# Kernel optimization log

Measured on AMD Instinct MI355X. Metric: run time of the kernel, lower is better.

The kernel has to match this reference:

```python
import jax, jax.numpy as jnp
import numpy as np

N = 100000   # nodes
E = 600000   # edges
F = 128      # input features
H = 128      # hidden size
A = 64       # n_actions
G = 64       # number of graphs in batch
L = 3        # GAT layers
EPS = 1e-5   # GraphNorm eps


def setup_inputs() -> dict:
    key = jax.random.key(0)
    ks = jax.random.split(key, 8)
    x = jax.random.normal(ks[0], (N, F), dtype=jnp.float32)
    edge_index = jax.random.randint(ks[1], (2, E), 0, N, dtype=jnp.int64)
    batch = jnp.sort(jax.random.randint(ks[2], (N,), 0, G, dtype=jnp.int64))
    Ws = jax.random.normal(ks[3], (L, H, H), dtype=jnp.float32) * (1.0 / np.sqrt(H))
    att_src = jax.random.normal(ks[4], (L, H), dtype=jnp.float32) * 0.1
    att_dst = jax.random.normal(ks[5], (L, H), dtype=jnp.float32) * 0.1
    conv_bias = jnp.zeros((L, H), dtype=jnp.float32)
    gn_weight = jnp.ones((L - 1, H), dtype=jnp.float32)
    gn_bias = jnp.zeros((L - 1, H), dtype=jnp.float32)
    gn_mean_scale = jnp.ones((L - 1, H), dtype=jnp.float32)
    W1 = jax.random.normal(ks[6], (H, H), dtype=jnp.float32) * (1.0 / np.sqrt(H))
    b1 = jnp.zeros((H,), dtype=jnp.float32)
    W2 = jax.random.normal(ks[7], (H, A), dtype=jnp.float32) * (1.0 / np.sqrt(H))
    b2 = jnp.zeros((A,), dtype=jnp.float32)
    return dict(x=x, edge_index=edge_index, batch=batch, Ws=Ws, att_src=att_src,
                att_dst=att_dst, conv_bias=conv_bias, gn_weight=gn_weight,
                gn_bias=gn_bias, gn_mean_scale=gn_mean_scale,
                W1=W1, b1=b1, W2=W2, b2=b2)


def reference(x, edge_index, batch, Ws, att_src, att_dst, conv_bias,
              gn_weight, gn_bias, gn_mean_scale, W1, b1, W2, b2):
    src, dst = edge_index[0], edge_index[1]
    n = x.shape[0]
    h = x
    for l in range(L):
        # GATConv (heads=1, add_self_loops=False): h' = W h, edge attention
        hW = h @ Ws[l]                              # [N,H]
        a_s = hW @ att_src[l]                       # [N]
        a_d = hW @ att_dst[l]                       # [N]
        e = jax.nn.leaky_relu(a_s[src] + a_d[dst], 0.2)      # [E]
        m = jax.ops.segment_max(e, dst, num_segments=n)      # stable softmax per dst
        ex = jnp.exp(e - m[dst])
        s = jax.ops.segment_sum(ex, dst, num_segments=n)
        alpha = ex / (s[dst] + 1e-16)               # PyG softmax eps
        h = jax.ops.segment_sum(hW[src] * alpha[:, None], dst, num_segments=n) + conv_bias[l]
        if l < L - 1:
            # GraphNorm with batch=None (source passes no batch to gnn): one graph
            mean = h.mean(axis=0, keepdims=True)
            out = h - mean * gn_mean_scale[l]
            var = (out * out).mean(axis=0, keepdims=True)
            h = gn_weight[l] * out / jnp.sqrt(var + EPS) + gn_bias[l]
            h = jax.nn.leaky_relu(h, 0.01)          # act between layers (not after last)
    pooled = jax.ops.segment_sum(h, batch, num_segments=G)   # global_add_pool [G,H]
    z = jax.nn.leaky_relu(pooled @ W1 + b1, 0.01)
    return z @ W2 + b2                               # [G,A]
```

## Files before the change

kernel.cpp:

```cpp
#include <hip/hip_runtime.h>
#include <math.h>

#define HD 128
#define GG 64
#define CSB 256

typedef __attribute__((ext_vector_type(8))) short short8;
typedef __attribute__((ext_vector_type(4))) float f32x4;

__device__ __forceinline__ float leaky(float x, float s) { return x > 0.f ? x : s * x; }

__device__ __forceinline__ unsigned short bf16_of(float f) {
    union { float f; unsigned u; } v; v.f = f;
    unsigned r = v.u + 0x7fffu + ((v.u >> 16) & 1u);
    return (unsigned short)(r >> 16);
}
__device__ __forceinline__ float f_of_bf16(unsigned short u) {
    union { unsigned u; float f; } v; v.u = ((unsigned)u) << 16;
    return v.f;
}

__device__ __forceinline__ int sw(int row, int chunk) {
    return row * 128 + ((chunk ^ (row & 15)) << 3);
}

__global__ void k_init(const float* __restrict__ Ws, unsigned short* __restrict__ Wt,
                       int* __restrict__ bcnt) {
    int i = blockIdx.x * 256 + threadIdx.x;
    if (i < 3 * 16384) {
        int l = i >> 14, rem = i & 16383;
        int nn = rem >> 7, k = rem & 127;
        Wt[i] = bf16_of(Ws[l * 16384 + k * 128 + nn]);
    }
    if (i < 513) bcnt[i] = 0;
}


__global__ __launch_bounds__(256) void k_gemm_a32(
    const float* __restrict__ A, const unsigned short* __restrict__ Wt,
    const float* __restrict__ att_s, const float* __restrict__ att_d,
    unsigned short* __restrict__ hWb, float* __restrict__ a_s, float* __restrict__ a_d,
    int n) {
    __shared__ unsigned short Bs[128 * 128];
    const int tid = threadIdx.x;
    const int base = blockIdx.x * 64;

    const uint4* Wt4 = (const uint4*)Wt;
    uint4* Bs4 = (uint4*)Bs;
#pragma unroll
    for (int j = 0; j < 8; ++j) {
        int flat = tid + j * 256;
        int col = flat >> 4, c8 = flat & 15;
        Bs4[(col << 4) + (c8 ^ (col & 15))] = Wt4[flat];
    }

    const int wave = tid >> 6, lane = tid & 63;
    const int m16 = lane & 15, quad = lane >> 4;

    short8 af[4];
    {
        int row = base + wave * 16 + m16;
        row = (row < n) ? row : (n - 1);
        const float4* ap = (const float4*)(A + (size_t)row * 128);
#pragma unroll
        for (int kk = 0; kk < 4; ++kk) {
            float4 v0 = ap[kk * 8 + quad * 2];
            float4 v1 = ap[kk * 8 + quad * 2 + 1];
            union { short8 s; unsigned u[4]; } P;
            P.u[0] = (unsigned)bf16_of(v0.x) | ((unsigned)bf16_of(v0.y) << 16);
            P.u[1] = (unsigned)bf16_of(v0.z) | ((unsigned)bf16_of(v0.w) << 16);
            P.u[2] = (unsigned)bf16_of(v1.x) | ((unsigned)bf16_of(v1.y) << 16);
            P.u[3] = (unsigned)bf16_of(v1.z) | ((unsigned)bf16_of(v1.w) << 16);
            af[kk] = P.s;
        }
    }
    __syncthreads();

    f32x4 acc[8];
#pragma unroll
    for (int ct = 0; ct < 8; ++ct) acc[ct] = (f32x4){0.f, 0.f, 0.f, 0.f};
#pragma unroll
    for (int kk = 0; kk < 4; ++kk) {
#pragma unroll
        for (int ct = 0; ct < 8; ++ct) {
            short8 bfr = *(const short8*)&Bs[sw(ct * 16 + m16, kk * 4 + quad)];
            acc[ct] = __builtin_amdgcn_mfma_f32_16x16x32_bf16(af[kk], bfr, acc[ct], 0, 0, 0);
        }
    }

#pragma unroll
    for (int reg = 0; reg < 4; ++reg) {
        int gr = base + wave * 16 + quad * 4 + reg;
        bool ok = gr < n;
        unsigned short* rowp = hWb + (size_t)gr * 128 + m16;
        float s = 0.f, dd = 0.f;
#pragma unroll
        for (int ct = 0; ct < 8; ++ct) {
            float v = acc[ct][reg];
            int col = ct * 16 + m16;
            if (ok) rowp[ct * 16] = bf16_of(v);
            s = fmaf(v, att_s[col], s);
            dd = fmaf(v, att_d[col], dd);
        }
#pragma unroll
        for (int off = 1; off < 16; off <<= 1) {
            s += __shfl_xor(s, off, 64);
            dd += __shfl_xor(dd, off, 64);
        }
        if (m16 == 0 && ok) { a_s[gr] = s; a_d[gr] = dd; }
    }
}

__global__ __launch_bounds__(256) void k_gemm_a16(
    const unsigned short* __restrict__ Ab, const unsigned short* __restrict__ Wt,
    const float* __restrict__ att_s, const float* __restrict__ att_d,
    const float* __restrict__ alpha, const float* __restrict__ beta,
    unsigned short* __restrict__ hWb, float* __restrict__ a_s, float* __restrict__ a_d,
    int n) {
    __shared__ unsigned short Bs[128 * 128];
    const int tid = threadIdx.x;
    const int base = blockIdx.x * 64;

    const uint4* Wt4 = (const uint4*)Wt;
    uint4* Bs4 = (uint4*)Bs;
#pragma unroll
    for (int j = 0; j < 8; ++j) {
        int flat = tid + j * 256;
        int col = flat >> 4, c8 = flat & 15;
        Bs4[(col << 4) + (c8 ^ (col & 15))] = Wt4[flat];
    }

    const int wave = tid >> 6, lane = tid & 63;
    const int m16 = lane & 15, quad = lane >> 4;
    const float4* al4 = (const float4*)alpha;
    const float4* be4 = (const float4*)beta;

    short8 af[4];
    {
        int row = base + wave * 16 + m16;
        row = (row < n) ? row : (n - 1);
        const uint4* ap = (const uint4*)(Ab + (size_t)row * 128);
#pragma unroll
        for (int kk = 0; kk < 4; ++kk) {
            uint4 raw = ap[kk * 4 + quad];
            int c4 = kk * 8 + quad * 2;
            float4 a0 = al4[c4], a1 = al4[c4 + 1];
            float4 b0 = be4[c4], b1 = be4[c4 + 1];
            float f0 = leaky(fmaf(f_of_bf16(raw.x & 0xffff), a0.x, b0.x), 0.01f);
            float f1 = leaky(fmaf(f_of_bf16(raw.x >> 16),    a0.y, b0.y), 0.01f);
            float f2 = leaky(fmaf(f_of_bf16(raw.y & 0xffff), a0.z, b0.z), 0.01f);
            float f3 = leaky(fmaf(f_of_bf16(raw.y >> 16),    a0.w, b0.w), 0.01f);
            float f4 = leaky(fmaf(f_of_bf16(raw.z & 0xffff), a1.x, b1.x), 0.01f);
            float f5 = leaky(fmaf(f_of_bf16(raw.z >> 16),    a1.y, b1.y), 0.01f);
            float f6 = leaky(fmaf(f_of_bf16(raw.w & 0xffff), a1.z, b1.z), 0.01f);
            float f7 = leaky(fmaf(f_of_bf16(raw.w >> 16),    a1.w, b1.w), 0.01f);
            union { short8 s; unsigned u[4]; } P;
            P.u[0] = (unsigned)bf16_of(f0) | ((unsigned)bf16_of(f1) << 16);
            P.u[1] = (unsigned)bf16_of(f2) | ((unsigned)bf16_of(f3) << 16);
            P.u[2] = (unsigned)bf16_of(f4) | ((unsigned)bf16_of(f5) << 16);
            P.u[3] = (unsigned)bf16_of(f6) | ((unsigned)bf16_of(f7) << 16);
            af[kk] = P.s;
        }
    }
    __syncthreads();

    f32x4 acc[8];
#pragma unroll
    for (int ct = 0; ct < 8; ++ct) acc[ct] = (f32x4){0.f, 0.f, 0.f, 0.f};
#pragma unroll
    for (int kk = 0; kk < 4; ++kk) {
#pragma unroll
        for (int ct = 0; ct < 8; ++ct) {
            short8 bfr = *(const short8*)&Bs[sw(ct * 16 + m16, kk * 4 + quad)];
            acc[ct] = __builtin_amdgcn_mfma_f32_16x16x32_bf16(af[kk], bfr, acc[ct], 0, 0, 0);
        }
    }

#pragma unroll
    for (int reg = 0; reg < 4; ++reg) {
        int gr = base + wave * 16 + quad * 4 + reg;
        bool ok = gr < n;
        unsigned short* rowp = hWb + (size_t)gr * 128 + m16;
        float s = 0.f, dd = 0.f;
#pragma unroll
        for (int ct = 0; ct < 8; ++ct) {
            float v = acc[ct][reg];
            int col = ct * 16 + m16;
            if (ok) rowp[ct * 16] = bf16_of(v);
            s = fmaf(v, att_s[col], s);
            dd = fmaf(v, att_d[col], dd);
        }
#pragma unroll
        for (int off = 1; off < 16; off <<= 1) {
            s += __shfl_xor(s, off, 64);
            dd += __shfl_xor(dd, off, 64);
        }
        if (m16 == 0 && ok) { a_s[gr] = s; a_d[gr] = dd; }
    }
}


__global__ __launch_bounds__(256) void k_bcount(const int* __restrict__ dst,
                                                int* __restrict__ bcnt, int e) {
    __shared__ int lh[512];
    const int tid = threadIdx.x;
    for (int t = tid; t < 512; t += 256) lh[t] = 0;
    __syncthreads();
    for (int i = blockIdx.x * 256 + tid; i < e; i += gridDim.x * 256)
        atomicAdd(&lh[dst[i] >> 9], 1);
    __syncthreads();
    for (int t = tid; t < 512; t += 256)
        if (lh[t]) atomicAdd(&bcnt[t], lh[t]);
}

__global__ void k_bscan(const int* __restrict__ bcnt, int* __restrict__ bbase,
                        int* __restrict__ bcur, int* __restrict__ offs,
                        int nbk, int n, int e) {
    __shared__ int s[512];
    int t = threadIdx.x;
    int v = (t < nbk) ? bcnt[t] : 0;
    s[t] = v;
    __syncthreads();
    for (int off = 1; off < 512; off <<= 1) {
        int u = (t >= off) ? s[t - off] : 0;
        __syncthreads();
        s[t] += u;
        __syncthreads();
    }
    if (t < nbk) { bbase[t] = s[t] - v; bcur[t] = s[t] - v; }
    if (t == 0) { bbase[nbk] = e; offs[n] = e; }
}

__global__ __launch_bounds__(256) void k_part(const int* __restrict__ src,
                                              const int* __restrict__ dst,
                                              int* __restrict__ bcur,
                                              int* __restrict__ ebuf, int e) {
    __shared__ int lh[512];
    __shared__ int lbase[512];
    const int tid = threadIdx.x;
    const int chunk = (e + gridDim.x - 1) / gridDim.x;
    const int i0 = blockIdx.x * chunk;
    const int i1 = min(e, i0 + chunk);
    for (int t = tid; t < 512; t += 256) lh[t] = 0;
    __syncthreads();
    for (int i = i0 + tid; i < i1; i += 256) atomicAdd(&lh[dst[i] >> 9], 1);
    __syncthreads();
    for (int t = tid; t < 512; t += 256) {
        int c = lh[t];
        lbase[t] = c ? atomicAdd(&bcur[t], c) : 0;
    }
    __syncthreads();
    for (int t = tid; t < 512; t += 256) lh[t] = 0;
    __syncthreads();
    for (int i = i0 + tid; i < i1; i += 256) {
        int d = dst[i];
        int b = d >> 9;
        int p = lbase[b] + atomicAdd(&lh[b], 1);
        ebuf[p] = ((d & 511) << 18) | src[i];
    }
}

__global__ __launch_bounds__(256) void k_bscatter(const int* __restrict__ ebuf,
                                                  const int* __restrict__ bbase,
                                                  int* __restrict__ offs,
                                                  int* __restrict__ esrc, int n) {
    const int b = blockIdx.x;
    const int tid = threadIdx.x;
    const int nb0 = b << 9;
    const int e0 = bbase[b], e1 = bbase[b + 1];
    __shared__ int cnt[512];
    __shared__ int sc[512];
    __shared__ int pos[512];
    for (int t = tid; t < 512; t += 256) cnt[t] = 0;
    __syncthreads();
    for (int i = e0 + tid; i < e1; i += 256) atomicAdd(&cnt[ebuf[i] >> 18], 1);
    __syncthreads();
    for (int t = tid; t < 512; t += 256) sc[t] = cnt[t];
    __syncthreads();
    for (int off = 1; off < 512; off <<= 1) {
        int t0 = tid, t1 = tid + 256;
        int v0 = (t0 >= off) ? sc[t0 - off] : 0;
        int v1 = sc[t1 - off];
        __syncthreads();
        sc[t0] += v0;
        sc[t1] += v1;
        __syncthreads();
    }
    for (int t = tid; t < 512; t += 256) pos[t] = e0 + sc[t] - cnt[t];
    __syncthreads();
    for (int t = tid; t < 512; t += 256) {
        int node = nb0 + t;
        if (node < n) offs[node] = pos[t];
    }
    __syncthreads();
    for (int i = e0 + tid; i < e1; i += 256) {
        int v = ebuf[i];
        int l = v >> 18;
        int p = atomicAdd(&pos[l], 1);
        esrc[p] = v & 0x3FFFF;
    }
}

__global__ __launch_bounds__(256) void k_agg(const unsigned short* __restrict__ hWb,
                                             const int* __restrict__ offs,
                                             const int* __restrict__ esrc,
                                             const float* __restrict__ a_s,
                                             const float* __restrict__ a_d,
                                             const float* __restrict__ bias,
                                             unsigned short* __restrict__ hb, int n) {
    int d = blockIdx.x * 4 + (threadIdx.x >> 6);
    int lane = threadIdx.x & 63;
    int q = lane >> 4;
    int l16 = lane & 15;
    if (d >= n) return;
    int p0 = offs[d], p1 = offs[d + 1];
    float ad = a_d[d];
    const uint4* hW8 = (const uint4*)hWb;
    float acc[8] = {0.f, 0.f, 0.f, 0.f, 0.f, 0.f, 0.f, 0.f};
    float ssum = 0.f;
    int s_cur = (p0 + q < p1) ? esrc[p0 + q] : 0;
    for (int p = p0 + q; p < p1; p += 4) {
        int s = s_cur;
        if (p + 4 < p1) s_cur = esrc[p + 4];
        float e = leaky(a_s[s] + ad, 0.2f);
        float ex = __expf(e);
        ssum += ex;
        uint4 raw = hW8[(size_t)s * 16 + l16];
        acc[0] = fmaf(ex, f_of_bf16(raw.x & 0xffff), acc[0]);
        acc[1] = fmaf(ex, f_of_bf16(raw.x >> 16),    acc[1]);
        acc[2] = fmaf(ex, f_of_bf16(raw.y & 0xffff), acc[2]);
        acc[3] = fmaf(ex, f_of_bf16(raw.y >> 16),    acc[3]);
        acc[4] = fmaf(ex, f_of_bf16(raw.z & 0xffff), acc[4]);
        acc[5] = fmaf(ex, f_of_bf16(raw.z >> 16),    acc[5]);
        acc[6] = fmaf(ex, f_of_bf16(raw.w & 0xffff), acc[6]);
        acc[7] = fmaf(ex, f_of_bf16(raw.w >> 16),    acc[7]);
    }
    ssum += __shfl_xor(ssum, 16, 64);
    ssum += __shfl_xor(ssum, 32, 64);
#pragma unroll
    for (int k = 0; k < 8; ++k) {
        acc[k] += __shfl_xor(acc[k], 16, 64);
        acc[k] += __shfl_xor(acc[k], 32, 64);
    }
    if (lane < 16) {
        float inv = 1.f / (ssum + 1e-16f);
        const float4* b4p = (const float4*)bias;
        float4 bb0 = b4p[l16 * 2], bb1 = b4p[l16 * 2 + 1];
        uint4 o;
        o.x = (unsigned)bf16_of(fmaf(acc[0], inv, bb0.x)) |
              ((unsigned)bf16_of(fmaf(acc[1], inv, bb0.y)) << 16);
        o.y = (unsigned)bf16_of(fmaf(acc[2], inv, bb0.z)) |
              ((unsigned)bf16_of(fmaf(acc[3], inv, bb0.w)) << 16);
        o.z = (unsigned)bf16_of(fmaf(acc[4], inv, bb1.x)) |
              ((unsigned)bf16_of(fmaf(acc[5], inv, bb1.y)) << 16);
        o.w = (unsigned)bf16_of(fmaf(acc[6], inv, bb1.z)) |
              ((unsigned)bf16_of(fmaf(acc[7], inv, bb1.w)) << 16);
        ((uint4*)hb)[(size_t)d * 16 + l16] = o;
    }
}

__global__ __launch_bounds__(256) void k_colstat6(const unsigned short* __restrict__ hb,
                                                  float* __restrict__ part, int n) {
    const uint4* h8 = (const uint4*)hb;
    const int tid = threadIdx.x;
    const int total = n * 16;
    float s[8] = {0.f,0.f,0.f,0.f,0.f,0.f,0.f,0.f};
    float q[8] = {0.f,0.f,0.f,0.f,0.f,0.f,0.f,0.f};
    for (int i = blockIdx.x * 256 + tid; i < total; i += CSB * 256) {
        uint4 raw = h8[i];
        float v0 = f_of_bf16(raw.x & 0xffff), v1 = f_of_bf16(raw.x >> 16);
        float v2 = f_of_bf16(raw.y & 0xffff), v3 = f_of_bf16(raw.y >> 16);
        float v4 = f_of_bf16(raw.z & 0xffff), v5 = f_of_bf16(raw.z >> 16);
        float v6 = f_of_bf16(raw.w & 0xffff), v7 = f_of_bf16(raw.w >> 16);
        s[0] += v0; q[0] = fmaf(v0, v0, q[0]);
        s[1] += v1; q[1] = fmaf(v1, v1, q[1]);
        s[2] += v2; q[2] = fmaf(v2, v2, q[2]);
        s[3] += v3; q[3] = fmaf(v3, v3, q[3]);
        s[4] += v4; q[4] = fmaf(v4, v4, q[4]);
        s[5] += v5; q[5] = fmaf(v5, v5, q[5]);
        s[6] += v6; q[6] = fmaf(v6, v6, q[6]);
        s[7] += v7; q[7] = fmaf(v7, v7, q[7]);
    }
    __shared__ float ss[256][9];
    __shared__ float sq[256][9];
#pragma unroll
    for (int k = 0; k < 8; ++k) { ss[tid][k] = s[k]; sq[tid][k] = q[k]; }
    __syncthreads();
    if (tid < 128) {
        int c = tid >> 3, k = tid & 7;
        float S = 0.f, Q = 0.f;
#pragma unroll
        for (int g = 0; g < 16; ++g) {
            S += ss[g * 16 + c][k];
            Q += sq[g * 16 + c][k];
        }
        part[blockIdx.x * 256 + tid] = S;
        part[blockIdx.x * 256 + 128 + tid] = Q;
    }
}

__global__ __launch_bounds__(256) void k_colfin(const float* __restrict__ part,
                                                const float* __restrict__ w,
                                                const float* __restrict__ bb,
                                                const float* __restrict__ ms,
                                                float* __restrict__ alpha,
                                                float* __restrict__ beta, float inv_n) {
    int tid = threadIdx.x;
    float a0 = 0.f, a1 = 0.f, a2 = 0.f, a3 = 0.f;
    for (int b = 0; b < CSB; b += 4) {
        a0 += part[(b + 0) * 256 + tid];
        a1 += part[(b + 1) * 256 + tid];
        a2 += part[(b + 2) * 256 + tid];
        a3 += part[(b + 3) * 256 + tid];
    }
    __shared__ float fin[256];
    fin[tid] = (a0 + a1) + (a2 + a3);
    __syncthreads();
    if (tid < 128) {
        float mean = fin[tid] * inv_n;
        float ex2 = fin[128 + tid] * inv_n;
        float m2 = mean * ms[tid];
        float var = ex2 - 2.f * m2 * mean + m2 * m2;
        float a = w[tid] * rsqrtf(var + 1e-5f);
        alpha[tid] = a;
        beta[tid] = bb[tid] - m2 * a;
    }
}

__device__ __forceinline__ int lower_bound_i(const int* __restrict__ a, int n, int key) {
    int lo = 0, hi = n;
    while (lo < hi) {
        int mid = (lo + hi) >> 1;
        if (a[mid] < key) lo = mid + 1; else hi = mid;
    }
    return lo;
}

__global__ __launch_bounds__(256) void k_pool(const unsigned short* __restrict__ hb,
                                              const int* __restrict__ batch,
                                              float* __restrict__ pooled4, int n) {
    int g = blockIdx.x >> 2, t4 = blockIdx.x & 3;
    int lo = lower_bound_i(batch, n, g);
    int hi = lower_bound_i(batch, n, g + 1);
    int len = hi - lo;
    int q = (len + 3) >> 2;
    int r0 = lo + t4 * q;
    int r1 = min(r0 + q, hi);
    int c4 = threadIdx.x & 31, rg = threadIdx.x >> 5;
    const ushort4* h4 = (const ushort4*)hb;
    float4 acc = make_float4(0.f, 0.f, 0.f, 0.f);
    for (int r = r0 + rg; r < r1; r += 8) {
        ushort4 hv = h4[(size_t)r * 32 + c4];
        acc.x += f_of_bf16(hv.x);
        acc.y += f_of_bf16(hv.y);
        acc.z += f_of_bf16(hv.z);
        acc.w += f_of_bf16(hv.w);
    }
    __shared__ float4 sred[256];
    sred[threadIdx.x] = acc;
    __syncthreads();
    if (threadIdx.x < 32) {
        float4 S = sred[threadIdx.x];
#pragma unroll
        for (int k = 1; k < 8; ++k) {
            float4 a = sred[threadIdx.x + 32 * k];
            S.x += a.x; S.y += a.y; S.z += a.z; S.w += a.w;
        }
        ((float4*)pooled4)[(t4 * GG + g) * 32 + threadIdx.x] = S;
    }
}

__global__ __launch_bounds__(128) void k_mlp(const float* __restrict__ pooled4,
                                             const float* __restrict__ W1,
                                             const float* __restrict__ b1,
                                             const float* __restrict__ W2,
                                             const float* __restrict__ b2,
                                             float* __restrict__ out) {
    __shared__ float pr[HD];
    __shared__ float zs[HD];
    int g = blockIdx.x, t = threadIdx.x;
    float pv = 0.f;
#pragma unroll
    for (int k = 0; k < 4; ++k) pv += pooled4[(k * GG + g) * HD + t];
    pr[t] = pv;
    __syncthreads();
    float acc = b1[t];
#pragma unroll 8
    for (int k = 0; k < HD; ++k) acc = fmaf(pr[k], W1[k * HD + t], acc);
    zs[t] = leaky(acc, 0.01f);
    __syncthreads();
    if (t < 64) {
        float a2 = b2[t];
#pragma unroll 8
        for (int k = 0; k < HD; ++k) a2 = fmaf(zs[k], W2[k * 64 + t], a2);
        out[g * 64 + t] = a2;
    }
}

extern "C" void kernel_launch(void* const* d_in, const int* in_sizes, int n_in,
                              void* d_out, int out_size, void* d_ws, size_t ws_size,
                              hipStream_t stream) {
    const float* x        = (const float*)d_in[0];
    const int*   ei       = (const int*)d_in[1];
    const int*   batch    = (const int*)d_in[2];
    const float* Ws       = (const float*)d_in[3];
    const float* att_src  = (const float*)d_in[4];
    const float* att_dst  = (const float*)d_in[5];
    const float* conv_bias= (const float*)d_in[6];
    const float* gn_w     = (const float*)d_in[7];
    const float* gn_b     = (const float*)d_in[8];
    const float* gn_ms    = (const float*)d_in[9];
    const float* W1       = (const float*)d_in[10];
    const float* b1       = (const float*)d_in[11];
    const float* W2       = (const float*)d_in[12];
    const float* b2       = (const float*)d_in[13];
    float* out = (float*)d_out;

    const int n = in_sizes[2];
    const int e = in_sizes[1] / 2;
    const int* src = ei;
    const int* dst = ei + e;
    const int nbk = (n + 511) >> 9;

    char* ws = (char*)d_ws;
    unsigned short* hWb = (unsigned short*)ws;
    unsigned short* hb  = hWb + (size_t)n * HD;
    float* a_s    = (float*)(hb + (size_t)n * HD);
    float* a_d    = a_s + n;
    float* alpha  = a_d + n;
    float* beta   = alpha + HD;
    float* pooled4= beta + HD;
    float* part   = pooled4 + 4 * GG * HD;
    unsigned short* Wt = (unsigned short*)(part + CSB * 256);
    int* offs     = (int*)(Wt + 3 * 16384);
    int* esrc     = offs + n + 1;
    int* ebuf     = esrc + e;
    int* bcnt     = ebuf + e;
    int* bbase    = bcnt + 513;
    int* bcur     = bbase + 514;

    k_init<<<192, 256, 0, stream>>>(Ws, Wt, bcnt);
    k_bcount<<<256, 256, 0, stream>>>(dst, bcnt, e);
    k_bscan<<<1, 512, 0, stream>>>(bcnt, bbase, bcur, offs, nbk, n, e);
    k_part<<<256, 256, 0, stream>>>(src, dst, bcur, ebuf, e);
    k_bscatter<<<nbk, 256, 0, stream>>>(ebuf, bbase, offs, esrc, n);

    for (int l = 0; l < 3; ++l) {
        if (l == 0) {
            k_gemm_a32<<<(n + 63) / 64, 256, 0, stream>>>(
                x, Wt, att_src, att_dst, hWb, a_s, a_d, n);
        } else {
            k_gemm_a16<<<(n + 63) / 64, 256, 0, stream>>>(
                hb, Wt + l * 16384, att_src + l * HD, att_dst + l * HD,
                alpha, beta, hWb, a_s, a_d, n);
        }
        k_agg<<<(n + 3) / 4, 256, 0, stream>>>(hWb, offs, esrc, a_s, a_d,
                                               conv_bias + l * HD, hb, n);
        if (l < 2) {
            k_colstat6<<<CSB, 256, 0, stream>>>(hb, part, n);
            k_colfin<<<1, 256, 0, stream>>>(part, gn_w + l * HD, gn_b + l * HD,
                                            gn_ms + l * HD, alpha, beta, 1.0f / n);
        }
    }

    k_pool<<<4 * GG, 256, 0, stream>>>(hb, batch, pooled4, n);
    k_mlp<<<GG, HD, 0, stream>>>(pooled4, W1, b1, W2, b2, out);
}
```

Measured before the change: 380.1 us.

## Assign one 16-lane group per destination node in aggregation, prefetch next edge

The aggregation kernel now gives each destination node a 16-lane group instead of a full 64-lane wave split into four edge streams. This removes the cross-quarter shuffle reduction and the idle lanes during the final write. The edge loop software-prefetches the next source row and its attention score, and the bf16 accumulation uses packed two-wide float FMAs. In exchange each group walks its edges serially, so there is less memory-level parallelism per node and more divergence when neighbouring nodes have different degrees.

```diff
diff --git a/kernel.cpp b/kernel.cpp
--- a/kernel.cpp
+++ b/kernel.cpp
@@ -7,6 +7,7 @@
 
 typedef __attribute__((ext_vector_type(8))) short short8;
 typedef __attribute__((ext_vector_type(4))) float f32x4;
+typedef __attribute__((ext_vector_type(2))) float f32x2;
 
 __device__ __forceinline__ float leaky(float x, float s) { return x > 0.f ? x : s * x; }
 
@@ -308,55 +309,55 @@
                                              const float* __restrict__ a_d,
                                              const float* __restrict__ bias,
                                              unsigned short* __restrict__ hb, int n) {
-    int d = blockIdx.x * 4 + (threadIdx.x >> 6);
-    int lane = threadIdx.x & 63;
-    int q = lane >> 4;
-    int l16 = lane & 15;
+    const int tid = threadIdx.x;
+    const int l16 = tid & 15;
+    const int d = blockIdx.x * 16 + (tid >> 4);
     if (d >= n) return;
-    int p0 = offs[d], p1 = offs[d + 1];
-    float ad = a_d[d];
+    const int p0 = offs[d], p1 = offs[d + 1];
+    const float ad = a_d[d];
     const uint4* hW8 = (const uint4*)hWb;
-    float acc[8] = {0.f, 0.f, 0.f, 0.f, 0.f, 0.f, 0.f, 0.f};
+
+    f32x2 acc0 = {0.f, 0.f}, acc1 = {0.f, 0.f}, acc2 = {0.f, 0.f}, acc3 = {0.f, 0.f};
     float ssum = 0.f;
-    int s_cur = (p0 + q < p1) ? esrc[p0 + q] : 0;
-    for (int p = p0 + q; p < p1; p += 4) {
-        int s = s_cur;
-        if (p + 4 < p1) s_cur = esrc[p + 4];
-        float e = leaky(a_s[s] + ad, 0.2f);
-        float ex = __expf(e);
+
+    int s_cur = (p0 < p1) ? esrc[p0] : 0;
+    uint4 raw = hW8[(size_t)s_cur * 16 + l16];
+    float as_cur = a_s[s_cur];
+    for (int p = p0; p < p1; ++p) {
+        const uint4 r = raw;
+        const float e = leaky(as_cur + ad, 0.2f);
+        const int pn = (p + 1 < p1) ? p + 1 : p;
+        const int s_nxt = esrc[pn];
+        raw = hW8[(size_t)s_nxt * 16 + l16];
+        as_cur = a_s[s_nxt];
+
+        const float ex = __expf(e);
         ssum += ex;
-        uint4 raw = hW8[(size_t)s * 16 + l16];
-        acc[0] = fmaf(ex, f_of_bf16(raw.x & 0xffff), acc[0]);
-        acc[1] = fmaf(ex, f_of_bf16(raw.x >> 16),    acc[1]);
-        acc[2] = fmaf(ex, f_of_bf16(raw.y & 0xffff), acc[2]);
-        acc[3] = fmaf(ex, f_of_bf16(raw.y >> 16),    acc[3]);
-        acc[4] = fmaf(ex, f_of_bf16(raw.z & 0xffff), acc[4]);
-        acc[5] = fmaf(ex, f_of_bf16(raw.z >> 16),    acc[5]);
-        acc[6] = fmaf(ex, f_of_bf16(raw.w & 0xffff), acc[6]);
-        acc[7] = fmaf(ex, f_of_bf16(raw.w >> 16),    acc[7]);
-    }
-    ssum += __shfl_xor(ssum, 16, 64);
-    ssum += __shfl_xor(ssum, 32, 64);
-#pragma unroll
-    for (int k = 0; k < 8; ++k) {
-        acc[k] += __shfl_xor(acc[k], 16, 64);
-        acc[k] += __shfl_xor(acc[k], 32, 64);
-    }
-    if (lane < 16) {
-        float inv = 1.f / (ssum + 1e-16f);
-        const float4* b4p = (const float4*)bias;
-        float4 bb0 = b4p[l16 * 2], bb1 = b4p[l16 * 2 + 1];
-        uint4 o;
-        o.x = (unsigned)bf16_of(fmaf(acc[0], inv, bb0.x)) |
-              ((unsigned)bf16_of(fmaf(acc[1], inv, bb0.y)) << 16);
-        o.y = (unsigned)bf16_of(fmaf(acc[2], inv, bb0.z)) |
-              ((unsigned)bf16_of(fmaf(acc[3], inv, bb0.w)) << 16);
-        o.z = (unsigned)bf16_of(fmaf(acc[4], inv, bb1.x)) |
-              ((unsigned)bf16_of(fmaf(acc[5], inv, bb1.y)) << 16);
-        o.w = (unsigned)bf16_of(fmaf(acc[6], inv, bb1.z)) |
-              ((unsigned)bf16_of(fmaf(acc[7], inv, bb1.w)) << 16);
-        ((uint4*)hb)[(size_t)d * 16 + l16] = o;
-    }
+        const f32x2 exv = {ex, ex};
+        f32x2 v;
+        v.x = f_of_bf16(r.x & 0xffff); v.y = f_of_bf16(r.x >> 16);
+        acc0 = __builtin_elementwise_fma(exv, v, acc0);
+        v.x = f_of_bf16(r.y & 0xffff); v.y = f_of_bf16(r.y >> 16);
+        acc1 = __builtin_elementwise_fma(exv, v, acc1);
+        v.x = f_of_bf16(r.z & 0xffff); v.y = f_of_bf16(r.z >> 16);
+        acc2 = __builtin_elementwise_fma(exv, v, acc2);
+        v.x = f_of_bf16(r.w & 0xffff); v.y = f_of_bf16(r.w >> 16);
+        acc3 = __builtin_elementwise_fma(exv, v, acc3);
+    }
+
+    const float inv = 1.f / (ssum + 1e-16f);
+    const float4* b4p = (const float4*)bias;
+    const float4 bb0 = b4p[l16 * 2], bb1 = b4p[l16 * 2 + 1];
+    uint4 o;
+    o.x = (unsigned)bf16_of(fmaf(acc0.x, inv, bb0.x)) |
+          ((unsigned)bf16_of(fmaf(acc0.y, inv, bb0.y)) << 16);
+    o.y = (unsigned)bf16_of(fmaf(acc1.x, inv, bb0.z)) |
+          ((unsigned)bf16_of(fmaf(acc1.y, inv, bb0.w)) << 16);
+    o.z = (unsigned)bf16_of(fmaf(acc2.x, inv, bb1.x)) |
+          ((unsigned)bf16_of(fmaf(acc2.y, inv, bb1.y)) << 16);
+    o.w = (unsigned)bf16_of(fmaf(acc3.x, inv, bb1.z)) |
+          ((unsigned)bf16_of(fmaf(acc3.y, inv, bb1.w)) << 16);
+    ((uint4*)hb)[(size_t)d * 16 + l16] = o;
 }
 
 __global__ __launch_bounds__(256) void k_colstat6(const unsigned short* __restrict__ hb,
@@ -554,8 +555,8 @@
                 hb, Wt + l * 16384, att_src + l * HD, att_dst + l * HD,
                 alpha, beta, hWb, a_s, a_d, n);
         }
-        k_agg<<<(n + 3) / 4, 256, 0, stream>>>(hWb, offs, esrc, a_s, a_d,
-                                               conv_bias + l * HD, hb, n);
+        k_agg<<<(n + 15) / 16, 256, 0, stream>>>(hWb, offs, esrc, a_s, a_d,
+                                                 conv_bias + l * HD, hb, n);
         if (l < 2) {
             k_colstat6<<<CSB, 256, 0, stream>>>(hb, part, n);
             k_colfin<<<1, 256, 0, stream>>>(part, gn_w + l * HD, gn_b + l * HD,
```

New measurement: 357.6 us. -5.9%, faster.
